# Performance work log

Measured on AMD Instinct MI355X. Metric: run time of the kernel, lower is better.

## Reference

```python
import jax, jax.numpy as jnp
import numpy as np

ALPHA = 0.2  # leaky relu slope
NEG = -9e15  # mask fill value from the torch code


def gat_layer(x, adj_mask, W, a):
    """One dense GAT attention head.
    Equivalent math to the torch layer, without materializing the
    [N, N, 2F] a_input tensor: a^T [h_i ; h_j] = (h @ a1)_i + (h @ a2)_j.
    x: [N, Fin], adj_mask: [N, N] bool, W: [Fin, Fout], a: [2*Fout, 1].
    """
    h = x @ W                              # [N, Fout]
    Fo = W.shape[1]
    s_src = h @ a[:Fo, 0]                  # [N]
    s_dst = h @ a[Fo:, 0]                  # [N]
    e = jax.nn.leaky_relu(s_src[:, None] + s_dst[None, :], ALPHA)  # [N, N]
    e = jnp.where(adj_mask, e, NEG)
    attn = jax.nn.softmax(e, axis=1)       # dropout is a no-op in eval mode
    return attn @ h                        # [N, Fout]


def setup_inputs() -> dict:
    key = jax.random.key(0)
    ks = jax.random.split(key, 6)
    N, nfeat, nhid, nclass, nheads = 4096, 512, 64, 32, 8
    x = jax.random.normal(ks[0], (N, nfeat), dtype=jnp.float32)
    adj = jax.random.randint(ks[1], (N, N), 0, 2, dtype=jnp.int32)
    # params scaled like torch uniform(-1/sqrt(fan_in), 1/sqrt(fan_in))
    W_att = jax.random.normal(ks[2], (nheads, nfeat, nhid), dtype=jnp.float32) / np.sqrt(nfeat)
    a_att = jax.random.normal(ks[3], (nheads, 2 * nhid, 1), dtype=jnp.float32) / np.sqrt(2 * nhid)
    W_out = jax.random.normal(ks[4], (nhid * nheads, nclass), dtype=jnp.float32) / np.sqrt(nhid * nheads)
    a_out = jax.random.normal(ks[5], (2 * nclass, 1), dtype=jnp.float32) / np.sqrt(2 * nclass)
    return {"x": x, "adj": adj, "W_att": W_att, "a_att": a_att,
            "W_out": W_out, "a_out": a_out}


def reference(x, adj, W_att, a_att, W_out, a_out):
    adj_mask = adj > 0  # [N, N]
    # multi-head layer, concat=True => elu per head, concat along features
    heads = jax.vmap(lambda W, a: jax.nn.elu(gat_layer(x, adj_mask, W, a)))(W_att, a_att)  # [H, N, nhid]
    H, N, Fh = heads.shape
    hcat = jnp.transpose(heads, (1, 0, 2)).reshape(N, H * Fh)  # [N, H*nhid]
    # output layer, concat=False, then elu applied by GAT.forward
    out = jax.nn.elu(gat_layer(hcat, adj_mask, W_out, a_out))  # [N, nclass]
    return out
```

## Files before the change

### kernel.cpp

```cpp
#include <hip/hip_runtime.h>
#include <math.h>

#define NN 4096
#define CC 512
#define MB (1024*1024)
#define LOG2E 1.4426950408889634f

typedef __attribute__((ext_vector_type(8))) __bf16 bf16x8;
typedef __attribute__((ext_vector_type(4))) float f32x4;
typedef unsigned short ushort_t;
typedef unsigned int uint_t;
typedef unsigned char uchar_t;

#if __has_builtin(__builtin_amdgcn_exp2f)
#define EXP2(x) __builtin_amdgcn_exp2f(x)
#else
#define EXP2(x) exp2f(x)
#endif

static __device__ __forceinline__ float elu1(float x){ return x > 0.f ? x : (__expf(x)-1.f); }
static __device__ __forceinline__ ushort_t f2bf(float f){
    union { float f; uint_t u; } v; v.f = f;
    uint_t r = (v.u + 0x7FFFu + ((v.u >> 16) & 1u)) >> 16;
    return (ushort_t)r;
}
static __device__ __forceinline__ float bf2f(ushort_t h){
    union { uint_t u; float f; } q; q.u = ((uint_t)h) << 16; return q.f;
}

__global__ void k_prepare(const float* __restrict__ x, const int* __restrict__ adj,
                          const float* __restrict__ Watt, const float* __restrict__ Wout,
                          ushort_t* __restrict__ xh, ushort_t* __restrict__ xl,
                          uint_t* __restrict__ abits,
                          ushort_t* __restrict__ Wh, ushort_t* __restrict__ Wl,
                          ushort_t* __restrict__ Wth, ushort_t* __restrict__ Wtl){
    const int bid = blockIdx.x;
    if (bid < 2048){
        int idx = bid*256 + threadIdx.x;
        float4 v = *(const float4*)&x[(size_t)idx*4];
        ushort4 h4, l4;
        h4.x = f2bf(v.x); h4.y = f2bf(v.y); h4.z = f2bf(v.z); h4.w = f2bf(v.w);
        l4.x = f2bf(v.x-bf2f(h4.x)); l4.y = f2bf(v.y-bf2f(h4.y));
        l4.z = f2bf(v.z-bf2f(h4.z)); l4.w = f2bf(v.w-bf2f(h4.w));
        *(ushort4*)&xh[(size_t)idx*4] = h4;
        *(ushort4*)&xl[(size_t)idx*4] = l4;
    } else if (bid < 4096){
        int idx = (bid-2048)*256 + threadIdx.x;
        int i = idx >> 7, q = idx & 127;
        const int4* p = (const int4*)&adj[(size_t)i*NN + q*32];
        uint_t m = 0;
        #pragma unroll
        for(int g=0; g<8; g++){
            int4 v = p[g];
            m |= (uint_t)(v.x > 0) << (g*4 + 0);
            m |= (uint_t)(v.y > 0) << (g*4 + 1);
            m |= (uint_t)(v.z > 0) << (g*4 + 2);
            m |= (uint_t)(v.w > 0) << (g*4 + 3);
        }
        abits[idx] = m;
    } else {
        int idx = (bid-4096)*256 + threadIdx.x;
        if (idx < 512*128){
            int c = idx >> 7, k = (idx & 127)*4;
            ushort4 h4, l4;
            float v[4];
            #pragma unroll
            for(int j=0;j<4;j++)
                v[j] = Watt[(c>>6)*(512*64) + (k+j)*64 + (c&63)];
            h4.x = f2bf(v[0]); h4.y = f2bf(v[1]); h4.z = f2bf(v[2]); h4.w = f2bf(v[3]);
            l4.x = f2bf(v[0]-bf2f(h4.x)); l4.y = f2bf(v[1]-bf2f(h4.y));
            l4.z = f2bf(v[2]-bf2f(h4.z)); l4.w = f2bf(v[3]-bf2f(h4.w));
            *(ushort4*)&Wh[(size_t)c*512 + k] = h4;
            *(ushort4*)&Wl[(size_t)c*512 + k] = l4;
        } else if (idx < 512*128 + 32*128){
            int idx2 = idx - 512*128;
            int n = idx2 >> 7, k = (idx2 & 127)*4;
            ushort4 h4, l4;
            float v[4];
            #pragma unroll
            for(int j=0;j<4;j++)
                v[j] = Wout[(size_t)(k+j)*32 + n];
            h4.x = f2bf(v[0]); h4.y = f2bf(v[1]); h4.z = f2bf(v[2]); h4.w = f2bf(v[3]);
            l4.x = f2bf(v[0]-bf2f(h4.x)); l4.y = f2bf(v[1]-bf2f(h4.y));
            l4.z = f2bf(v[2]-bf2f(h4.z)); l4.w = f2bf(v[3]-bf2f(h4.w));
            *(ushort4*)&Wth[(size_t)n*512 + k] = h4;
            *(ushort4*)&Wtl[(size_t)n*512 + k] = l4;
        }
    }
}

__global__ __launch_bounds__(256) void k_gemm1(
        const ushort_t* __restrict__ xh, const ushort_t* __restrict__ xl,
        const ushort_t* __restrict__ Wh, const ushort_t* __restrict__ Wl,
        const float* __restrict__ aatt,
        ushort_t* __restrict__ hT,
        float* __restrict__ ssrc2, float* __restrict__ sdst2){
    const int t = threadIdx.x;
    const int l = t & 63, wv = t >> 6;
    const int lr = l & 15, lg = l >> 4;
    const int ib = blockIdx.x*64 + wv*16;
    const int hd = blockIdx.y;
    const int j0 = hd*64;

    f32x4 acc[4] = {};
    #pragma unroll 2
    for(int ks=0; ks<16; ks++){
        const int kb = ks*32 + lg*8;
        bf16x8 ah = *(const bf16x8*)&xh[(size_t)(ib+lr)*512 + kb];
        bf16x8 al = *(const bf16x8*)&xl[(size_t)(ib+lr)*512 + kb];
        bf16x8 bh[4], bl[4];
        #pragma unroll
        for(int nt=0;nt<4;nt++){
            bh[nt] = *(const bf16x8*)&Wh[(size_t)(j0+nt*16+lr)*512 + kb];
            bl[nt] = *(const bf16x8*)&Wl[(size_t)(j0+nt*16+lr)*512 + kb];
        }
        #pragma unroll
        for(int nt=0;nt<4;nt++){
            acc[nt] = __builtin_amdgcn_mfma_f32_16x16x32_bf16(ah, bh[nt], acc[nt], 0,0,0);
            acc[nt] = __builtin_amdgcn_mfma_f32_16x16x32_bf16(al, bh[nt], acc[nt], 0,0,0);
            acc[nt] = __builtin_amdgcn_mfma_f32_16x16x32_bf16(ah, bl[nt], acc[nt], 0,0,0);
        }
    }
    #pragma unroll
    for(int nt=0;nt<4;nt++){
        const int col = j0 + nt*16 + lr;
        ushort4 o;
        o.x = f2bf(acc[nt][0]); o.y = f2bf(acc[nt][1]);
        o.z = f2bf(acc[nt][2]); o.w = f2bf(acc[nt][3]);
        *(ushort4*)&hT[(size_t)col*NN + ib + lg*4] = o;
    }
    float a1v[4], a2v[4];
    #pragma unroll
    for(int nt=0;nt<4;nt++){
        a1v[nt] = aatt[hd*128 + nt*16 + lr];
        a2v[nt] = aatt[hd*128 + 64 + nt*16 + lr];
    }
    #pragma unroll
    for(int r=0;r<4;r++){
        float ps = acc[0][r]*a1v[0] + acc[1][r]*a1v[1] + acc[2][r]*a1v[2] + acc[3][r]*a1v[3];
        float pd = acc[0][r]*a2v[0] + acc[1][r]*a2v[1] + acc[2][r]*a2v[2] + acc[3][r]*a2v[3];
        #pragma unroll
        for(int m=1;m<16;m<<=1){
            ps += __shfl_xor(ps, m);
            pd += __shfl_xor(pd, m);
        }
        if (lr == 0){
            ssrc2[hd*NN + ib + lg*4 + r] = ps*LOG2E;
            sdst2[hd*NN + ib + lg*4 + r] = pd*LOG2E;
        }
    }
}

__global__ __launch_bounds__(256) void k_attn1(
        const ushort_t* __restrict__ hT,
        const float* __restrict__ ssrc2, const float* __restrict__ sdst2,
        const uchar_t* __restrict__ abits,
        ushort_t* __restrict__ hch, ushort_t* __restrict__ hcl){
    const int t = threadIdx.x;
    const int l = t & 63, wv = t >> 6;
    const int hd = blockIdx.y;
    const int i0 = blockIdx.x*32;
    const int lr = l & 15, lg = l >> 4;

    f32x4 acc[2][4] = {};
    f32x4 dacc[2] = {};

    float ss[2];
    #pragma unroll
    for(int mh=0;mh<2;mh++)
        ss[mh] = ssrc2[hd*NN + i0 + mh*16 + lr];

    bf16x8 ones;
    #pragma unroll
    for(int e=0;e<8;e++) ones[e] = (__bf16)1.0f;

    const int jwb = wv*1024;
    const uchar_t* arow[2];
    #pragma unroll
    for(int mh=0;mh<2;mh++)
        arow[mh] = &abits[(size_t)(i0 + mh*16 + lr)*512 + (jwb >> 3)];

    bf16x8 bA[4], bB[4];
    float4 sdaA, sdbA, sdaB, sdbB;
    uint_t bitsA[2], bitsB[2];

#define LOAD1(SFX, JT) { \
    const int jb_ = jwb + (JT)*32 + lg*8; \
    _Pragma("unroll") \
    for(int nt=0;nt<4;nt++) \
        b##SFX[nt] = *(const bf16x8*)&hT[(size_t)(hd*64 + nt*16 + lr)*NN + jb_]; \
    sda##SFX = *(const float4*)&sdst2[hd*NN + jb_]; \
    sdb##SFX = *(const float4*)&sdst2[hd*NN + jb_ + 4]; \
    _Pragma("unroll") \
    for(int mh=0;mh<2;mh++) \
        bits##SFX[mh] = arow[mh][(JT)*4 + lg]; }

#define COMP1(SFX) { \
    float sdv[8] = {sda##SFX.x, sda##SFX.y, sda##SFX.z, sda##SFX.w, \
                    sdb##SFX.x, sdb##SFX.y, sdb##SFX.z, sdb##SFX.w}; \
    _Pragma("unroll") \
    for(int mh=0;mh<2;mh++){ \
        const uint_t bits = bits##SFX[mh]; \
        bf16x8 a; \
        _Pragma("unroll") \
        for(int e=0;e<8;e++){ \
            float s_ = ss[mh] + sdv[e]; \
            float t_ = fmaxf(s_, 0.2f*s_); \
            float w_ = EXP2(t_) * (float)((bits >> e) & 1u); \
            a[e] = (__bf16)w_; \
        } \
        _Pragma("unroll") \
        for(int nt=0;nt<4;nt++) \
            acc[mh][nt] = __builtin_amdgcn_mfma_f32_16x16x32_bf16( \
                a, b##SFX[nt], acc[mh][nt], 0, 0, 0); \
        dacc[mh] = __builtin_amdgcn_mfma_f32_16x16x32_bf16( \
                a, ones, dacc[mh], 0, 0, 0); \
    } }

    LOAD1(A, 0);
    for(int jt=0; jt<32; jt+=2){
        LOAD1(B, jt+1);
        COMP1(A);
        if (jt + 2 < 32) LOAD1(A, jt+2);
        COMP1(B);
    }
#undef LOAD1
#undef COMP1

    __shared__ f32x4 red[4][10][64];
    #pragma unroll
    for(int mh=0;mh<2;mh++){
        #pragma unroll
        for(int nt=0;nt<4;nt++) red[wv][mh*5+nt][l] = acc[mh][nt];
        red[wv][mh*5+4][l] = dacc[mh];
    }
    __syncthreads();
    if (wv < 2){
        const int mh = wv;
        f32x4 s[4], dd;
        #pragma unroll
        for(int nt=0;nt<4;nt++)
            s[nt] = red[0][mh*5+nt][l] + red[1][mh*5+nt][l]
                  + red[2][mh*5+nt][l] + red[3][mh*5+nt][l];
        dd = red[0][mh*5+4][l] + red[1][mh*5+4][l]
           + red[2][mh*5+4][l] + red[3][mh*5+4][l];
        #pragma unroll
        for(int nt=0;nt<4;nt++){
            const int col = hd*64 + nt*16 + lr;
            #pragma unroll
            for(int r=0;r<4;r++){
                const int row = i0 + mh*16 + lg*4 + r;
                float v_ = elu1(s[nt][r] / dd[r]);
                ushort_t hi_ = f2bf(v_);
                hch[(size_t)row*512 + col] = hi_;
                hcl[(size_t)row*512 + col] = f2bf(v_ - bf2f(hi_));
            }
        }
    }
}

__global__ __launch_bounds__(256) void k_gemm2(
        const ushort_t* __restrict__ hch, const ushort_t* __restrict__ hcl,
        const ushort_t* __restrict__ Wth, const ushort_t* __restrict__ Wtl,
        const float* __restrict__ aout,
        ushort_t* __restrict__ h2T, float* __restrict__ ss2, float* __restrict__ sd2){
    const int t = threadIdx.x;
    const int l = t & 63, wv = t >> 6;
    const int lr = l & 15, lg = l >> 4;
    const int ib = blockIdx.x*64 + wv*16;

    f32x4 acc[2] = {};
    #pragma unroll 2
    for(int ks=0; ks<16; ks++){
        const int kb = ks*32 + lg*8;
        bf16x8 ah = *(const bf16x8*)&hch[(size_t)(ib+lr)*512 + kb];
        bf16x8 al = *(const bf16x8*)&hcl[(size_t)(ib+lr)*512 + kb];
        bf16x8 bh[2], bl[2];
        #pragma unroll
        for(int nt=0;nt<2;nt++){
            bh[nt] = *(const bf16x8*)&Wth[(size_t)(nt*16+lr)*512 + kb];
            bl[nt] = *(const bf16x8*)&Wtl[(size_t)(nt*16+lr)*512 + kb];
        }
        #pragma unroll
        for(int nt=0;nt<2;nt++){
            acc[nt] = __builtin_amdgcn_mfma_f32_16x16x32_bf16(ah, bh[nt], acc[nt], 0,0,0);
            acc[nt] = __builtin_amdgcn_mfma_f32_16x16x32_bf16(al, bh[nt], acc[nt], 0,0,0);
            acc[nt] = __builtin_amdgcn_mfma_f32_16x16x32_bf16(ah, bl[nt], acc[nt], 0,0,0);
        }
    }
    #pragma unroll
    for(int nt=0;nt<2;nt++)
        #pragma unroll
        for(int r=0;r<4;r++)
            h2T[(size_t)(nt*16+lr)*NN + ib + lg*4 + r] = f2bf(acc[nt][r]);
    float a1v[2], a2v[2];
    #pragma unroll
    for(int nt=0;nt<2;nt++){
        a1v[nt] = aout[nt*16 + lr];
        a2v[nt] = aout[32 + nt*16 + lr];
    }
    #pragma unroll
    for(int r=0;r<4;r++){
        float ps = acc[0][r]*a1v[0] + acc[1][r]*a1v[1];
        float pd = acc[0][r]*a2v[0] + acc[1][r]*a2v[1];
        #pragma unroll
        for(int m=1;m<16;m<<=1){
            ps += __shfl_xor(ps, m);
            pd += __shfl_xor(pd, m);
        }
        if (lr == 0){
            ss2[ib + lg*4 + r] = ps*LOG2E;
            sd2[ib + lg*4 + r] = pd*LOG2E;
        }
    }
}

__global__ __launch_bounds__(256) void k_attn2(
        const ushort_t* __restrict__ h2T,
        const float* __restrict__ ss2, const float* __restrict__ sd2,
        const uchar_t* __restrict__ abits,
        float* __restrict__ pnum2T, float* __restrict__ pden2){
    const int t = threadIdx.x;
    const int l = t & 63, wv = t >> 6;
    const int i0 = blockIdx.x*64;
    const int jc = blockIdx.y;
    const int lr = l & 15, lg = l >> 4;

    f32x4 acc[4][2] = {};
    f32x4 dacc[4] = {};

    float ss[4];
    #pragma unroll
    for(int mh=0;mh<4;mh++)
        ss[mh] = ss2[i0 + mh*16 + lr];

    bf16x8 ones;
    #pragma unroll
    for(int e=0;e<8;e++) ones[e] = (__bf16)1.0f;

    const int jwb = jc*512 + wv*128;
    const uchar_t* arow[4];
    #pragma unroll
    for(int mh=0;mh<4;mh++)
        arow[mh] = &abits[(size_t)(i0 + mh*16 + lr)*512 + (jwb >> 3)];

    bf16x8 bA[2], bB[2];
    float4 sdaA, sdbA, sdaB, sdbB;
    uint_t bitsA[4], bitsB[4];

#define LOAD2(SFX, JT) { \
    const int jb_ = jwb + (JT)*32 + lg*8; \
    _Pragma("unroll") \
    for(int nt=0;nt<2;nt++) \
        b##SFX[nt] = *(const bf16x8*)&h2T[(size_t)(nt*16 + lr)*NN + jb_]; \
    sda##SFX = *(const float4*)&sd2[jb_]; \
    sdb##SFX = *(const float4*)&sd2[jb_ + 4]; \
    _Pragma("unroll") \
    for(int mh=0;mh<4;mh++) \
        bits##SFX[mh] = arow[mh][(JT)*4 + lg]; }

#define COMP2(SFX) { \
    float sdv[8] = {sda##SFX.x, sda##SFX.y, sda##SFX.z, sda##SFX.w, \
                    sdb##SFX.x, sdb##SFX.y, sdb##SFX.z, sdb##SFX.w}; \
    _Pragma("unroll") \
    for(int mh=0;mh<4;mh++){ \
        const uint_t bits = bits##SFX[mh]; \
        bf16x8 a; \
        _Pragma("unroll") \
        for(int e=0;e<8;e++){ \
            float s_ = ss[mh] + sdv[e]; \
            float t_ = fmaxf(s_, 0.2f*s_); \
            float w_ = EXP2(t_) * (float)((bits >> e) & 1u); \
            a[e] = (__bf16)w_; \
        } \
        _Pragma("unroll") \
        for(int nt=0;nt<2;nt++) \
            acc[mh][nt] = __builtin_amdgcn_mfma_f32_16x16x32_bf16( \
                a, b##SFX[nt], acc[mh][nt], 0, 0, 0); \
        dacc[mh] = __builtin_amdgcn_mfma_f32_16x16x32_bf16( \
                a, ones, dacc[mh], 0, 0, 0); \
    } }

    LOAD2(A, 0);
    for(int jt=0; jt<4; jt+=2){
        LOAD2(B, jt+1);
        COMP2(A);
        if (jt + 2 < 4) LOAD2(A, jt+2);
        COMP2(B);
    }
#undef LOAD2
#undef COMP2

    __shared__ f32x4 red2[2][12][64];
    __syncthreads();
    if (wv >= 2){
        #pragma unroll
        for(int mh=0;mh<4;mh++){
            #pragma unroll
            for(int nt=0;nt<2;nt++) red2[wv-2][mh*2+nt][l] = acc[mh][nt];
            red2[wv-2][8+mh][l] = dacc[mh];
        }
    }
    __syncthreads();
    if (wv < 2){
        #pragma unroll
        for(int mh=0;mh<4;mh++){
            #pragma unroll
            for(int nt=0;nt<2;nt++) acc[mh][nt] += red2[wv][mh*2+nt][l];
            dacc[mh] += red2[wv][8+mh][l];
        }
    }
    __syncthreads();
    if (wv == 1){
        #pragma unroll
        for(int mh=0;mh<4;mh++){
            #pragma unroll
            for(int nt=0;nt<2;nt++) red2[0][mh*2+nt][l] = acc[mh][nt];
            red2[0][8+mh][l] = dacc[mh];
        }
    }
    __syncthreads();
    if (wv == 0){
        #pragma unroll
        for(int mh=0;mh<4;mh++){
            #pragma unroll
            for(int nt=0;nt<2;nt++){
                f32x4 v = acc[mh][nt] + red2[0][mh*2+nt][l];
                int col = nt*16 + lr;
                float4 o = {v[0], v[1], v[2], v[3]};
                *(float4*)&pnum2T[((size_t)jc*32 + col)*NN + i0 + mh*16 + lg*4] = o;
            }
            f32x4 d = dacc[mh] + red2[0][8+mh][l];
            if (lr == 0){
                #pragma unroll
                for(int r=0;r<4;r++)
                    pden2[(size_t)jc*NN + i0 + mh*16 + lg*4 + r] = d[r];
            }
        }
    }
}

__global__ void k_reduce2(const float* __restrict__ pnum2T, const float* __restrict__ pden2,
                          float* __restrict__ out){
    int idx = blockIdx.x*256 + threadIdx.x;
    int c = idx >> 10, i4 = (idx & 1023)*4;
    f32x4 s = {}, d = {};
    #pragma unroll
    for(int jc=0;jc<8;jc++){
        s += *(const f32x4*)&pnum2T[((size_t)jc*32 + c)*NN + i4];
        d += *(const f32x4*)&pden2[(size_t)jc*NN + i4];
    }
    #pragma unroll
    for(int r=0;r<4;r++)
        out[(size_t)(i4+r)*32 + c] = elu1(s[r]/d[r]);
}

extern "C" void kernel_launch(void* const* d_in, const int* in_sizes, int n_in,
                              void* d_out, int out_size, void* d_ws, size_t ws_size,
                              hipStream_t stream){
    const float* x    = (const float*)d_in[0];
    const int*   adj  = (const int*)  d_in[1];
    const float* Watt = (const float*)d_in[2];
    const float* aatt = (const float*)d_in[3];
    const float* Wout = (const float*)d_in[4];
    const float* aout = (const float*)d_in[5];
    float* out = (float*)d_out;
    char* ws = (char*)d_ws;

    ushort_t* hch   = (ushort_t*)(ws + (size_t) 0*MB);
    ushort_t* hcl   = (ushort_t*)(ws + (size_t) 4*MB);
    ushort_t* Whi   = (ushort_t*)(ws + (size_t) 8*MB);
    ushort_t* Wlo   = (ushort_t*)(ws + (size_t) 8*MB + 512*1024);
    float*    ssrc2 = (float*)   (ws + (size_t) 9*MB);
    float*    sdst2 = (float*)   (ws + (size_t)10*MB);
    ushort_t* hT    = (ushort_t*)(ws + (size_t)11*MB);
    uint_t*   abits = (uint_t*)  (ws + (size_t)15*MB);
    ushort_t* Wth   = (ushort_t*)(ws + (size_t)17*MB);
    ushort_t* Wtl   = (ushort_t*)(ws + (size_t)17*MB + 64*1024);
    float*    ss2   = (float*)   (ws + (size_t)18*MB);
    float*    sd2   = (float*)   (ws + (size_t)19*MB);
    ushort_t* h2T   = (ushort_t*)(ws + (size_t)20*MB);
    float*    pden2 = (float*)   (ws + (size_t)21*MB);
    float*    pnum2T= (float*)   (ws + (size_t)22*MB);
    ushort_t* xh    = (ushort_t*)(ws + (size_t)26*MB);
    ushort_t* xl    = (ushort_t*)(ws + (size_t)30*MB);
    if (ws_size < (size_t)40*MB) return;

    k_prepare <<<4368, 256, 0, stream>>>(x, adj, Watt, Wout, xh, xl, abits,
                                         Whi, Wlo, Wth, Wtl);
    k_gemm1   <<<dim3(64,8), 256, 0, stream>>>(xh, xl, Whi, Wlo, aatt, hT, ssrc2, sdst2);
    k_attn1   <<<dim3(128,8), 256, 0, stream>>>(hT, ssrc2, sdst2, (const uchar_t*)abits, hch, hcl);
    k_gemm2   <<<64, 256, 0, stream>>>(hch, hcl, Wth, Wtl, aout, h2T, ss2, sd2);
    k_attn2   <<<dim3(64,8), 256, 0, stream>>>(h2T, ss2, sd2, (const uchar_t*)abits, pnum2T, pden2);
    k_reduce2 <<<128, 256, 0, stream>>>(pnum2T, pden2, out);
}
```

Measured before the change: 273.4 us.

## Split first attention over two j-chunks with 64-row tiles and separate reduce

The first-layer attention kernel now processes 64 rows per block and splits the neighbor dimension into two chunks across a new grid axis. Partial numerators and denominators go to global scratch, and a new reduce kernel combines them and applies ELU and the bf16 hi/lo split. The denominator is accumulated with scalar adds and cross-lane shuffles instead of an extra MFMA against a ones vector, and the kernel requests three blocks per CU. Each loaded hT tile is reused across more rows, at the cost of writing and re-reading a 16 MB fp32 partial buffer plus one more kernel launch.

```diff
diff --git a/kernel.cpp b/kernel.cpp
--- a/kernel.cpp
+++ b/kernel.cpp
@@ -151,38 +151,35 @@
     }
 }
 
-__global__ __launch_bounds__(256) void k_attn1(
+__global__ __launch_bounds__(256, 3) void k_attn1(
         const ushort_t* __restrict__ hT,
         const float* __restrict__ ssrc2, const float* __restrict__ sdst2,
         const uchar_t* __restrict__ abits,
-        ushort_t* __restrict__ hch, ushort_t* __restrict__ hcl){
+        float* __restrict__ pnum, float* __restrict__ pden){
     const int t = threadIdx.x;
     const int l = t & 63, wv = t >> 6;
-    const int hd = blockIdx.y;
-    const int i0 = blockIdx.x*32;
+    const int i0 = blockIdx.x*64;
+    const int jc = blockIdx.y;
+    const int hd = blockIdx.z;
     const int lr = l & 15, lg = l >> 4;
 
-    f32x4 acc[2][4] = {};
-    f32x4 dacc[2] = {};
-
-    float ss[2];
-    #pragma unroll
-    for(int mh=0;mh<2;mh++)
+    f32x4 acc[4][4] = {};
+    float den[4] = {0.f,0.f,0.f,0.f};
+
+    float ss[4];
+    #pragma unroll
+    for(int mh=0;mh<4;mh++)
         ss[mh] = ssrc2[hd*NN + i0 + mh*16 + lr];
 
-    bf16x8 ones;
-    #pragma unroll
-    for(int e=0;e<8;e++) ones[e] = (__bf16)1.0f;
-
-    const int jwb = wv*1024;
-    const uchar_t* arow[2];
-    #pragma unroll
-    for(int mh=0;mh<2;mh++)
+    const int jwb = jc*2048 + wv*512;
+    const uchar_t* arow[4];
+    #pragma unroll
+    for(int mh=0;mh<4;mh++)
         arow[mh] = &abits[(size_t)(i0 + mh*16 + lr)*512 + (jwb >> 3)];
 
     bf16x8 bA[4], bB[4];
     float4 sdaA, sdbA, sdaB, sdbB;
-    uint_t bitsA[2], bitsB[2];
+    uint_t bitsA[4], bitsB[4];
 
 #define LOAD1(SFX, JT) { \
     const int jb_ = jwb + (JT)*32 + lg*8; \
@@ -192,71 +189,91 @@
     sda##SFX = *(const float4*)&sdst2[hd*NN + jb_]; \
     sdb##SFX = *(const float4*)&sdst2[hd*NN + jb_ + 4]; \
     _Pragma("unroll") \
-    for(int mh=0;mh<2;mh++) \
+    for(int mh=0;mh<4;mh++) \
         bits##SFX[mh] = arow[mh][(JT)*4 + lg]; }
 
 #define COMP1(SFX) { \
     float sdv[8] = {sda##SFX.x, sda##SFX.y, sda##SFX.z, sda##SFX.w, \
                     sdb##SFX.x, sdb##SFX.y, sdb##SFX.z, sdb##SFX.w}; \
     _Pragma("unroll") \
-    for(int mh=0;mh<2;mh++){ \
+    for(int mh=0;mh<4;mh++){ \
         const uint_t bits = bits##SFX[mh]; \
         bf16x8 a; \
+        float dl = 0.f; \
         _Pragma("unroll") \
         for(int e=0;e<8;e++){ \
             float s_ = ss[mh] + sdv[e]; \
             float t_ = fmaxf(s_, 0.2f*s_); \
             float w_ = EXP2(t_) * (float)((bits >> e) & 1u); \
+            dl += w_; \
             a[e] = (__bf16)w_; \
         } \
+        den[mh] += dl; \
         _Pragma("unroll") \
         for(int nt=0;nt<4;nt++) \
             acc[mh][nt] = __builtin_amdgcn_mfma_f32_16x16x32_bf16( \
                 a, b##SFX[nt], acc[mh][nt], 0, 0, 0); \
-        dacc[mh] = __builtin_amdgcn_mfma_f32_16x16x32_bf16( \
-                a, ones, dacc[mh], 0, 0, 0); \
     } }
 
     LOAD1(A, 0);
-    for(int jt=0; jt<32; jt+=2){
+    for(int jt=0; jt<16; jt+=2){
         LOAD1(B, jt+1);
         COMP1(A);
-        if (jt + 2 < 32) LOAD1(A, jt+2);
+        if (jt + 2 < 16) LOAD1(A, jt+2);
         COMP1(B);
     }
 #undef LOAD1
 #undef COMP1
 
-    __shared__ f32x4 red[4][10][64];
-    #pragma unroll
-    for(int mh=0;mh<2;mh++){
-        #pragma unroll
-        for(int nt=0;nt<4;nt++) red[wv][mh*5+nt][l] = acc[mh][nt];
-        red[wv][mh*5+4][l] = dacc[mh];
-    }
-    __syncthreads();
-    if (wv < 2){
-        const int mh = wv;
-        f32x4 s[4], dd;
-        #pragma unroll
-        for(int nt=0;nt<4;nt++)
-            s[nt] = red[0][mh*5+nt][l] + red[1][mh*5+nt][l]
-                  + red[2][mh*5+nt][l] + red[3][mh*5+nt][l];
-        dd = red[0][mh*5+4][l] + red[1][mh*5+4][l]
-           + red[2][mh*5+4][l] + red[3][mh*5+4][l];
-        #pragma unroll
-        for(int nt=0;nt<4;nt++){
-            const int col = hd*64 + nt*16 + lr;
-            #pragma unroll
-            for(int r=0;r<4;r++){
-                const int row = i0 + mh*16 + lg*4 + r;
-                float v_ = elu1(s[nt][r] / dd[r]);
-                ushort_t hi_ = f2bf(v_);
-                hch[(size_t)row*512 + col] = hi_;
-                hcl[(size_t)row*512 + col] = f2bf(v_ - bf2f(hi_));
-            }
-        }
-    }
+    __shared__ f32x4 red[4][9][64];
+
+#define EPI(M0) { \
+    __syncthreads(); \
+    _Pragma("unroll") \
+    for(int m=0;m<2;m++) \
+        _Pragma("unroll") \
+        for(int nt=0;nt<4;nt++) red[wv][m*4+nt][l] = acc[(M0)+m][nt]; \
+    { f32x4 dv = {den[(M0)], den[(M0)+1], 0.f, 0.f}; red[wv][8][l] = dv; } \
+    __syncthreads(); \
+    if (wv < 2){ \
+        const int mh = (M0) + wv; \
+        f32x4 s4[4]; \
+        _Pragma("unroll") \
+        for(int nt=0;nt<4;nt++) \
+            s4[nt] = red[0][wv*4+nt][l] + red[1][wv*4+nt][l] \
+                   + red[2][wv*4+nt][l] + red[3][wv*4+nt][l]; \
+        f32x4 dv = red[0][8][l] + red[1][8][l] + red[2][8][l] + red[3][8][l]; \
+        float d = (wv == 0) ? dv[0] : dv[1]; \
+        d += __shfl_xor(d, 16); \
+        d += __shfl_xor(d, 32); \
+        if (lg == 0) \
+            pden[((size_t)jc*8 + hd)*NN + i0 + mh*16 + lr] = d; \
+        _Pragma("unroll") \
+        for(int nt=0;nt<4;nt++){ \
+            const int col = hd*64 + nt*16 + lr; \
+            _Pragma("unroll") \
+            for(int r=0;r<4;r++){ \
+                const int row = i0 + mh*16 + lg*4 + r; \
+                pnum[((size_t)jc*NN + row)*512 + col] = s4[nt][r]; \
+            } \
+        } \
+    } }
+
+    EPI(0);
+    EPI(2);
+#undef EPI
+}
+
+__global__ void k_reduce1(const float* __restrict__ pnum, const float* __restrict__ pden,
+                          ushort_t* __restrict__ hch, ushort_t* __restrict__ hcl){
+    int idx = blockIdx.x*256 + threadIdx.x;
+    int i = idx >> 9, c = idx & 511, hd = c >> 6;
+    float s = pnum[idx] + pnum[(size_t)NN*512 + idx];
+    float d = pden[(size_t)hd*NN + i] + pden[(size_t)(8 + hd)*NN + i];
+    float v = elu1(s/d);
+    ushort_t hi = f2bf(v);
+    hch[idx] = hi;
+    hcl[idx] = f2bf(v - bf2f(hi));
 }
 
 __global__ __launch_bounds__(256) void k_gemm2(
@@ -484,12 +501,15 @@
     float*    pnum2T= (float*)   (ws + (size_t)22*MB);
     ushort_t* xh    = (ushort_t*)(ws + (size_t)26*MB);
     ushort_t* xl    = (ushort_t*)(ws + (size_t)30*MB);
-    if (ws_size < (size_t)40*MB) return;
+    float*    pnum  = (float*)   (ws + (size_t)34*MB);
+    float*    pden  = (float*)   (ws + (size_t)50*MB);
+    if (ws_size < (size_t)51*MB) return;
 
     k_prepare <<<4368, 256, 0, stream>>>(x, adj, Watt, Wout, xh, xl, abits,
                                          Whi, Wlo, Wth, Wtl);
     k_gemm1   <<<dim3(64,8), 256, 0, stream>>>(xh, xl, Whi, Wlo, aatt, hT, ssrc2, sdst2);
-    k_attn1   <<<dim3(128,8), 256, 0, stream>>>(hT, ssrc2, sdst2, (const uchar_t*)abits, hch, hcl);
+    k_attn1   <<<dim3(64,2,8), 256, 0, stream>>>(hT, ssrc2, sdst2, (const uchar_t*)abits, pnum, pden);
+    k_reduce1 <<<8192, 256, 0, stream>>>(pnum, pden, hch, hcl);
     k_gemm2   <<<64, 256, 0, stream>>>(hch, hcl, Wth, Wtl, aout, h2T, ss2, sd2);
     k_attn2   <<<dim3(64,8), 256, 0, stream>>>(h2T, ss2, sd2, (const uchar_t*)abits, pnum2T, pden2);
     k_reduce2 <<<128, 256, 0, stream>>>(pnum2T, pden2, out);
```

Measured after the change: 367.3 us. +34.3%, slower.
